# Kernel optimization log

Measured on AMD Instinct MI355X. Metric: run time of the kernel, lower is better.

The kernel has to match this reference:

```python
import jax, jax.numpy as jnp
import numpy as np

N = 50000   # nodes
E = 800000  # edges (avg degree 16)
H = 4       # attention heads
NEG_SLOPE = 0.2


def gatv2_conv(h, src, dst, W, attn, act):
    """One DGL-style GATv2Conv with share_weights=True, no bias/residual.
    h: [N, Fin]; W: [Fin, H*D]; attn: [H, D].
    """
    n = h.shape[0]
    Hh, D = attn.shape
    feat = (h @ W).reshape(n, Hh, D)          # shared src/dst projection
    el = feat[src]                             # [E, H, D] gathered source feats
    er = feat[dst]                             # [E, H, D] gathered dest feats
    # GATv2 score: a^T leaky_relu(W h_i + W h_j)
    e = jnp.sum(jax.nn.leaky_relu(el + er, NEG_SLOPE) * attn, axis=-1)  # [E, H]
    # edge softmax over incoming edges of each destination node
    m = jax.ops.segment_max(e, dst, num_segments=n)        # [N, H]
    ex = jnp.exp(e - m[dst])                                # stable exp
    s = jax.ops.segment_sum(ex, dst, num_segments=n)        # [N, H]
    a = ex / s[dst]                                         # [E, H]
    # weighted scatter-sum of source features
    rst = jax.ops.segment_sum(el * a[:, :, None], dst, num_segments=n)  # [N, H, D]
    return act(rst) if act is not None else rst


def setup_inputs() -> dict:
    key = jax.random.key(0)
    ks = jax.random.split(key, 12)
    p = lambda k, shape: (jax.random.normal(k, shape, jnp.float32) * 0.1)
    return {
        "features": jax.random.normal(ks[0], (N, 16), jnp.float32),
        "W0": p(ks[3], (16, H * 32)),  "attn0": p(ks[4], (H, 32)),
        "W1": p(ks[5], (H * 32, H * 32)), "attn1": p(ks[6], (H, 32)),
        "W2": p(ks[7], (H * 32, H * 32)), "attn2": p(ks[8], (H, 32)),
        "W3": p(ks[9], (H * 32, H * 8)),  "attn3": p(ks[10], (H, 8)),
        "src": jax.random.randint(ks[1], (E,), 0, N, jnp.int32),
        "dst": jax.random.randint(ks[2], (E,), 0, N, jnp.int32),
    }


def reference(features, W0, attn0, W1, attn1, W2, attn2, W3, attn3, src, dst):
    h = gatv2_conv(features, src, dst, W0, attn0, jax.nn.elu).reshape(N, -1)
    h = gatv2_conv(h, src, dst, W1, attn1, jax.nn.elu).reshape(N, -1)
    h = gatv2_conv(h, src, dst, W2, attn2, jax.nn.elu).reshape(N, -1)
    logits = gatv2_conv(h, src, dst, W3, attn3, None).mean(axis=1)  # [N, num_classes]
    return logits
```

## Files before the change

### kernel.cpp

```cpp
#include <hip/hip_runtime.h>
#include <hip/hip_bf16.h>
#include <math.h>

#define N_NODES 50000
#define N_EDGES 800000
#define HEADS 4
#define NEG 0.2f

#define SCAN_TILE 1024
#define SCAN_NB ((N_NODES + SCAN_TILE - 1) / SCAN_TILE)

template<int FIN>
__global__ __launch_bounds__(256) void gemm128_kernel(const float* __restrict__ h,
                                                      const float* __restrict__ W,
                                                      float* __restrict__ out) {
    constexpr int ROWS = 32;
    __shared__ float hs[ROWS][FIN];
    const int tid = threadIdx.x;
    const int rbase = blockIdx.x * ROWS;
    constexpr int VECS = ROWS * FIN / 4;
    for (int i = tid; i < VECS; i += 256) {
        int r = (i * 4) / FIN, c = (i * 4) % FIN;
        int gr = rbase + r;
        float4 v = {0.f, 0.f, 0.f, 0.f};
        if (gr < N_NODES) v = *(const float4*)(h + (size_t)gr * FIN + c);
        *(float4*)(&hs[r][c]) = v;
    }
    __syncthreads();
    const int c4 = (tid & 31) * 4;
    const int r0 = (tid >> 5) * 4;
    float a0[4] = {}, a1[4] = {}, a2[4] = {}, a3[4] = {};
    for (int k = 0; k < FIN; ++k) {
        const float4 w = *(const float4*)(W + k * 128 + c4);
        const float h0 = hs[r0 + 0][k], h1 = hs[r0 + 1][k];
        const float h2 = hs[r0 + 2][k], h3 = hs[r0 + 3][k];
        a0[0] += h0 * w.x; a0[1] += h0 * w.y; a0[2] += h0 * w.z; a0[3] += h0 * w.w;
        a1[0] += h1 * w.x; a1[1] += h1 * w.y; a1[2] += h1 * w.z; a1[3] += h1 * w.w;
        a2[0] += h2 * w.x; a2[1] += h2 * w.y; a2[2] += h2 * w.z; a2[3] += h2 * w.w;
        a3[0] += h3 * w.x; a3[1] += h3 * w.y; a3[2] += h3 * w.z; a3[3] += h3 * w.w;
    }
    float* rows[4] = {a0, a1, a2, a3};
#pragma unroll
    for (int i = 0; i < 4; ++i) {
        int gr = rbase + r0 + i;
        if (gr < N_NODES) {
            float4 v = {rows[i][0], rows[i][1], rows[i][2], rows[i][3]};
            *(float4*)(out + (size_t)gr * 128 + c4) = v;
        }
    }
}

template<int FIN, int FOUT>
__global__ __launch_bounds__(128) void gemm_kernel(const float* __restrict__ h,
                                                   const float* __restrict__ W,
                                                   float* __restrict__ out) {
    constexpr int ROWS = 16;
    constexpr int SUBS = 128 / FOUT;
    constexpr int RPT  = ROWS / SUBS;
    __shared__ float hs[ROWS][FIN];
    const int tid = threadIdx.x;
    const int rbase = blockIdx.x * ROWS;
    for (int i = tid; i < ROWS * FIN; i += 128) {
        int r = i / FIN, c = i % FIN;
        int gr = rbase + r;
        hs[r][c] = (gr < N_NODES) ? h[(size_t)gr * FIN + c] : 0.f;
    }
    __syncthreads();
    const int col = tid % FOUT;
    const int sub = tid / FOUT;
    float acc[RPT];
#pragma unroll
    for (int i = 0; i < RPT; ++i) acc[i] = 0.f;
    for (int k = 0; k < FIN; ++k) {
        float w = W[k * FOUT + col];
#pragma unroll
        for (int i = 0; i < RPT; ++i) acc[i] += hs[sub * RPT + i][k] * w;
    }
#pragma unroll
    for (int i = 0; i < RPT; ++i) {
        int gr = rbase + sub * RPT + i;
        if (gr < N_NODES) out[(size_t)gr * FOUT + col] = acc[i];
    }
}

__global__ __launch_bounds__(256) void deg_count(const int* __restrict__ dst,
                                                 int* __restrict__ deg) {
    int e = blockIdx.x * blockDim.x + threadIdx.x;
    if (e < N_EDGES) atomicAdd(&deg[dst[e]], 1);
}

__global__ __launch_bounds__(256) void scan_reduce(const int* __restrict__ deg,
                                                   int* __restrict__ bsum) {
    __shared__ int wtot[4];
    const int tid = threadIdx.x;
    const int base = blockIdx.x * SCAN_TILE + tid * 4;
    int s = 0;
    if (base < N_NODES) {
        int4 v = *(const int4*)(deg + base);
        s = v.x + v.y + v.z + v.w;
    }
#pragma unroll
    for (int off = 1; off < 64; off <<= 1) s += __shfl_xor(s, off, 64);
    if ((tid & 63) == 0) wtot[tid >> 6] = s;
    __syncthreads();
    if (tid == 0) bsum[blockIdx.x] = wtot[0] + wtot[1] + wtot[2] + wtot[3];
}

__global__ __launch_bounds__(256) void scan_write(const int* __restrict__ deg,
                                                  const int* __restrict__ bsum,
                                                  int* __restrict__ row_ptr,
                                                  int* __restrict__ woff) {
    __shared__ int s_boff;
    __shared__ int wtot[4];
    const int tid  = threadIdx.x;
    const int lane = tid & 63;
    const int wid  = tid >> 6;
    const int b    = blockIdx.x;
    if (wid == 0) {
        int v = (lane < b) ? bsum[lane] : 0;
#pragma unroll
        for (int off = 1; off < 64; off <<= 1) v += __shfl_xor(v, off, 64);
        if (lane == 0) s_boff = v;
    }
    const int base = b * SCAN_TILE + tid * 4;
    int4 v = {0, 0, 0, 0};
    if (base < N_NODES) v = *(const int4*)(deg + base);
    const int t0 = v.x, t1 = t0 + v.y, t2 = t1 + v.z, t3 = t2 + v.w;
    int x = t3;
#pragma unroll
    for (int off = 1; off < 64; off <<= 1) {
        int t = __shfl_up(x, off, 64);
        if (lane >= off) x += t;
    }
    if (lane == 63) wtot[wid] = x;
    __syncthreads();
    int woffs = 0;
    for (int w = 0; w < wid; ++w) woffs += wtot[w];
    const int off0 = s_boff + woffs + (x - t3);
    if (base < N_NODES) {
        row_ptr[base + 1] = off0 + t0;  woff[base + 0] = off0 + t0 - v.x;
        row_ptr[base + 2] = off0 + t1;  woff[base + 1] = off0 + t1 - v.y;
        row_ptr[base + 3] = off0 + t2;  woff[base + 2] = off0 + t2 - v.z;
        row_ptr[base + 4] = off0 + t3;  woff[base + 3] = off0 + t3 - v.w;
    }
    if (b == 0 && tid == 0) row_ptr[0] = 0;
}

__global__ __launch_bounds__(256) void scatter_kernel(const int* __restrict__ src,
                                                      const int* __restrict__ dst,
                                                      int* __restrict__ woff,
                                                      int* __restrict__ csr_src) {
    int e = blockIdx.x * blockDim.x + threadIdx.x;
    if (e < N_EDGES) {
        int pos = atomicAdd(&woff[dst[e]], 1);
        csr_src[pos] = src[e];
    }
}

template<int D, int MODE>
__global__ __launch_bounds__(256) void fused_gat(const float* __restrict__ feat,
                                                 const int* __restrict__ row_ptr,
                                                 const int* __restrict__ csr_src,
                                                 const float* __restrict__ attn,
                                                 float* __restrict__ out) {
    constexpr int F   = HEADS * D;
    constexpr int LPN = F / 4;
    constexpr int NPW = 64 / LPN;
    const int lane = threadIdx.x & 63;
    const int wave = (blockIdx.x * blockDim.x + threadIdx.x) >> 6;
    const int sub  = lane / LPN;
    const int l    = lane % LPN;
    const int v    = wave * NPW + sub;
    if (v >= N_NODES) return;

    const float4 a4 = *(const float4*)(attn + (l * 4));
    const float4 fv = *(const float4*)(feat + (size_t)v * F + l * 4);

    float m = -INFINITY, s = 0.f;
    float4 acc = {0.f, 0.f, 0.f, 0.f};

    const int beg = row_ptr[v], end = row_ptr[v + 1];
    int j = beg;
    for (; j + 1 < end; j += 2) {
        const int u0 = csr_src[j], u1 = csr_src[j + 1];
        const float4 f0 = *(const float4*)(feat + (size_t)u0 * F + l * 4);
        const float4 f1 = *(const float4*)(feat + (size_t)u1 * F + l * 4);
        float t, sc0 = 0.f, sc1 = 0.f;
        t = f0.x + fv.x; t = t > 0.f ? t : t * NEG; sc0 += t * a4.x;
        t = f0.y + fv.y; t = t > 0.f ? t : t * NEG; sc0 += t * a4.y;
        t = f0.z + fv.z; t = t > 0.f ? t : t * NEG; sc0 += t * a4.z;
        t = f0.w + fv.w; t = t > 0.f ? t : t * NEG; sc0 += t * a4.w;
        t = f1.x + fv.x; t = t > 0.f ? t : t * NEG; sc1 += t * a4.x;
        t = f1.y + fv.y; t = t > 0.f ? t : t * NEG; sc1 += t * a4.y;
        t = f1.z + fv.z; t = t > 0.f ? t : t * NEG; sc1 += t * a4.z;
        t = f1.w + fv.w; t = t > 0.f ? t : t * NEG; sc1 += t * a4.w;
#pragma unroll
        for (int off = 1; off < D / 4; off <<= 1) {
            sc0 += __shfl_xor(sc0, off, 64);
            sc1 += __shfl_xor(sc1, off, 64);
        }
        const float scmax = fmaxf(sc0, sc1);
        if (scmax > m) {
            const float scale = __expf(m - scmax);
            s *= scale;
            acc.x *= scale; acc.y *= scale; acc.z *= scale; acc.w *= scale;
            m = scmax;
        }
        const float p0 = __expf(sc0 - m);
        const float p1 = __expf(sc1 - m);
        s += p0 + p1;
        acc.x += f0.x * p0 + f1.x * p1;
        acc.y += f0.y * p0 + f1.y * p1;
        acc.z += f0.z * p0 + f1.z * p1;
        acc.w += f0.w * p0 + f1.w * p1;
    }
    if (j < end) {
        const int u = csr_src[j];
        const float4 fu = *(const float4*)(feat + (size_t)u * F + l * 4);
        float t, sc = 0.f;
        t = fu.x + fv.x; t = t > 0.f ? t : t * NEG; sc += t * a4.x;
        t = fu.y + fv.y; t = t > 0.f ? t : t * NEG; sc += t * a4.y;
        t = fu.z + fv.z; t = t > 0.f ? t : t * NEG; sc += t * a4.z;
        t = fu.w + fv.w; t = t > 0.f ? t : t * NEG; sc += t * a4.w;
#pragma unroll
        for (int off = 1; off < D / 4; off <<= 1)
            sc += __shfl_xor(sc, off, 64);
        if (sc > m) {
            const float scale = __expf(m - sc);
            s *= scale;
            acc.x *= scale; acc.y *= scale; acc.z *= scale; acc.w *= scale;
            m = sc;
        }
        const float p = __expf(sc - m);
        s += p;
        acc.x += fu.x * p;
        acc.y += fu.y * p;
        acc.z += fu.z * p;
        acc.w += fu.w * p;
    }

    const float inv = (s > 0.f) ? 1.f / s : 0.f;
    float4 r;
    r.x = acc.x * inv; r.y = acc.y * inv; r.z = acc.z * inv; r.w = acc.w * inv;
    if (MODE == 0) {
        r.x = r.x > 0.f ? r.x : expm1f(r.x);
        r.y = r.y > 0.f ? r.y : expm1f(r.y);
        r.z = r.z > 0.f ? r.z : expm1f(r.z);
        r.w = r.w > 0.f ? r.w : expm1f(r.w);
        *(float4*)(out + (size_t)v * F + l * 4) = r;
    } else {
        r.x += __shfl_xor(r.x, 2, 64); r.y += __shfl_xor(r.y, 2, 64);
        r.z += __shfl_xor(r.z, 2, 64); r.w += __shfl_xor(r.w, 2, 64);
        r.x += __shfl_xor(r.x, 4, 64); r.y += __shfl_xor(r.y, 4, 64);
        r.z += __shfl_xor(r.z, 4, 64); r.w += __shfl_xor(r.w, 4, 64);
        if (l < 2) {
            r.x *= 0.25f; r.y *= 0.25f; r.z *= 0.25f; r.w *= 0.25f;
            *(float4*)(out + (size_t)v * 8 + l * 4) = r;
        }
    }
}

extern "C" void kernel_launch(void* const* d_in, const int* in_sizes, int n_in,
                              void* d_out, int out_size, void* d_ws, size_t ws_size,
                              hipStream_t stream) {
    const float* features = (const float*)d_in[0];
    const float* W0 = (const float*)d_in[1];  const float* attn0 = (const float*)d_in[2];
    const float* W1 = (const float*)d_in[3];  const float* attn1 = (const float*)d_in[4];
    const float* W2 = (const float*)d_in[5];  const float* attn2 = (const float*)d_in[6];
    const float* W3 = (const float*)d_in[7];  const float* attn3 = (const float*)d_in[8];
    const int* src = (const int*)d_in[9];
    const int* dst = (const int*)d_in[10];
    float* out = (float*)d_out;

    float* bufA   = (float*)d_ws;
    float* feat   = bufA + (size_t)N_NODES * 128;
    int* row_ptr  = (int*)(feat + (size_t)N_NODES * 128);
    int* woff     = row_ptr + (N_NODES + 1);
    int* deg      = woff + N_NODES;
    int* csr_src  = deg + N_NODES;
    int* bsum     = csr_src + N_EDGES;

    const int EBLK = (N_EDGES + 255) / 256;
    const int GB32 = (N_NODES + 31) / 32;
    const int GB16 = (N_NODES + 15) / 16;

    hipMemsetAsync(deg, 0, (size_t)N_NODES * 4, stream);
    deg_count<<<EBLK, 256, 0, stream>>>(dst, deg);
    scan_reduce<<<SCAN_NB, 256, 0, stream>>>(deg, bsum);
    scan_write<<<SCAN_NB, 256, 0, stream>>>(deg, bsum, row_ptr, woff);
    scatter_kernel<<<EBLK, 256, 0, stream>>>(src, dst, woff, csr_src);

    const int FB32 = ((N_NODES + 1) / 2 * 64 + 255) / 256;
    const int FB8  = ((N_NODES + 7) / 8 * 64 + 255) / 256;

    gemm128_kernel<16><<<GB32, 256, 0, stream>>>(features, W0, feat);
    fused_gat<32, 0><<<FB32, 256, 0, stream>>>(feat, row_ptr, csr_src, attn0, bufA);
    gemm128_kernel<128><<<GB32, 256, 0, stream>>>(bufA, W1, feat);
    fused_gat<32, 0><<<FB32, 256, 0, stream>>>(feat, row_ptr, csr_src, attn1, bufA);
    gemm128_kernel<128><<<GB32, 256, 0, stream>>>(bufA, W2, feat);
    fused_gat<32, 0><<<FB32, 256, 0, stream>>>(feat, row_ptr, csr_src, attn2, bufA);
    gemm_kernel<128, 32><<<GB16, 128, 0, stream>>>(bufA, W3, feat);
    fused_gat<8, 1><<<FB8, 256, 0, stream>>>(feat, row_ptr, csr_src, attn3, out);
}
```

Baseline: 467.9 us.

## Assign one wavefront per node and split edges across sub-slots with online-softmax merge

Each node now gets a full 64-lane wavefront instead of sharing one. The lanes are split into edge-parallel slots that each process a strided subset of incoming edges with unrolled loads. Partial online-softmax states (max, sum, accumulator) are then merged across slots with xor shuffles, and only slot 0 writes. The aim is more memory-level parallelism and shorter serial edge chains per node. In exchange it uses 2x (D=32) or 8x (D=8) more waves, plus extra merge shuffles and exps.

```diff
diff --git a/kernel.cpp b/kernel.cpp
--- a/kernel.cpp
+++ b/kernel.cpp
@@ -163,97 +163,113 @@
                                                  const int* __restrict__ csr_src,
                                                  const float* __restrict__ attn,
                                                  float* __restrict__ out) {
-    constexpr int F   = HEADS * D;
-    constexpr int LPN = F / 4;
-    constexpr int NPW = 64 / LPN;
+    constexpr int F    = HEADS * D;
+    constexpr int LPN  = F / 4;
+    constexpr int EPAR = 64 / LPN;
+    constexpr int UNR  = (D == 32) ? 4 : 2;
+    constexpr int CHUNK = EPAR * UNR;
     const int lane = threadIdx.x & 63;
-    const int wave = (blockIdx.x * blockDim.x + threadIdx.x) >> 6;
-    const int sub  = lane / LPN;
+    const int v    = (blockIdx.x * blockDim.x + threadIdx.x) >> 6;
+    if (v >= N_NODES) return;
+    const int slot = lane / LPN;
     const int l    = lane % LPN;
-    const int v    = wave * NPW + sub;
-    if (v >= N_NODES) return;
-
-    const float4 a4 = *(const float4*)(attn + (l * 4));
+
+    const float4 a4 = *(const float4*)(attn + l * 4);
     const float4 fv = *(const float4*)(feat + (size_t)v * F + l * 4);
 
     float m = -INFINITY, s = 0.f;
     float4 acc = {0.f, 0.f, 0.f, 0.f};
 
     const int beg = row_ptr[v], end = row_ptr[v + 1];
-    int j = beg;
-    for (; j + 1 < end; j += 2) {
-        const int u0 = csr_src[j], u1 = csr_src[j + 1];
-        const float4 f0 = *(const float4*)(feat + (size_t)u0 * F + l * 4);
-        const float4 f1 = *(const float4*)(feat + (size_t)u1 * F + l * 4);
-        float t, sc0 = 0.f, sc1 = 0.f;
-        t = f0.x + fv.x; t = t > 0.f ? t : t * NEG; sc0 += t * a4.x;
-        t = f0.y + fv.y; t = t > 0.f ? t : t * NEG; sc0 += t * a4.y;
-        t = f0.z + fv.z; t = t > 0.f ? t : t * NEG; sc0 += t * a4.z;
-        t = f0.w + fv.w; t = t > 0.f ? t : t * NEG; sc0 += t * a4.w;
-        t = f1.x + fv.x; t = t > 0.f ? t : t * NEG; sc1 += t * a4.x;
-        t = f1.y + fv.y; t = t > 0.f ? t : t * NEG; sc1 += t * a4.y;
-        t = f1.z + fv.z; t = t > 0.f ? t : t * NEG; sc1 += t * a4.z;
-        t = f1.w + fv.w; t = t > 0.f ? t : t * NEG; sc1 += t * a4.w;
+    for (int jc = beg; jc < end; jc += CHUNK) {
+        int    idx[UNR];
+        bool   act[UNR];
+        float4 fr[UNR];
+        float  sc[UNR];
+#pragma unroll
+        for (int u = 0; u < UNR; ++u) {
+            const int j = jc + u * EPAR + slot;
+            act[u] = (j < end);
+            idx[u] = act[u] ? csr_src[j] : v;
+        }
+#pragma unroll
+        for (int u = 0; u < UNR; ++u)
+            fr[u] = *(const float4*)(feat + (size_t)idx[u] * F + l * 4);
+#pragma unroll
+        for (int u = 0; u < UNR; ++u) {
+            float t, x;
+            t = fr[u].x + fv.x; t = t > 0.f ? t : t * NEG; x  = t * a4.x;
+            t = fr[u].y + fv.y; t = t > 0.f ? t : t * NEG; x += t * a4.y;
+            t = fr[u].z + fv.z; t = t > 0.f ? t : t * NEG; x += t * a4.z;
+            t = fr[u].w + fv.w; t = t > 0.f ? t : t * NEG; x += t * a4.w;
+            sc[u] = x;
+        }
 #pragma unroll
         for (int off = 1; off < D / 4; off <<= 1) {
-            sc0 += __shfl_xor(sc0, off, 64);
-            sc1 += __shfl_xor(sc1, off, 64);
-        }
-        const float scmax = fmaxf(sc0, sc1);
+#pragma unroll
+            for (int u = 0; u < UNR; ++u)
+                sc[u] += __shfl_xor(sc[u], off, 64);
+        }
+#pragma unroll
+        for (int u = 0; u < UNR; ++u)
+            if (!act[u]) sc[u] = -INFINITY;
+        float scmax = sc[0];
+#pragma unroll
+        for (int u = 1; u < UNR; ++u) scmax = fmaxf(scmax, sc[u]);
         if (scmax > m) {
             const float scale = __expf(m - scmax);
             s *= scale;
             acc.x *= scale; acc.y *= scale; acc.z *= scale; acc.w *= scale;
             m = scmax;
         }
-        const float p0 = __expf(sc0 - m);
-        const float p1 = __expf(sc1 - m);
-        s += p0 + p1;
-        acc.x += f0.x * p0 + f1.x * p1;
-        acc.y += f0.y * p0 + f1.y * p1;
-        acc.z += f0.z * p0 + f1.z * p1;
-        acc.w += f0.w * p0 + f1.w * p1;
-    }
-    if (j < end) {
-        const int u = csr_src[j];
-        const float4 fu = *(const float4*)(feat + (size_t)u * F + l * 4);
-        float t, sc = 0.f;
-        t = fu.x + fv.x; t = t > 0.f ? t : t * NEG; sc += t * a4.x;
-        t = fu.y + fv.y; t = t > 0.f ? t : t * NEG; sc += t * a4.y;
-        t = fu.z + fv.z; t = t > 0.f ? t : t * NEG; sc += t * a4.z;
-        t = fu.w + fv.w; t = t > 0.f ? t : t * NEG; sc += t * a4.w;
-#pragma unroll
-        for (int off = 1; off < D / 4; off <<= 1)
-            sc += __shfl_xor(sc, off, 64);
-        if (sc > m) {
-            const float scale = __expf(m - sc);
-            s *= scale;
-            acc.x *= scale; acc.y *= scale; acc.z *= scale; acc.w *= scale;
-            m = sc;
-        }
-        const float p = __expf(sc - m);
-        s += p;
-        acc.x += fu.x * p;
-        acc.y += fu.y * p;
-        acc.z += fu.z * p;
-        acc.w += fu.w * p;
+#pragma unroll
+        for (int u = 0; u < UNR; ++u) {
+            const float p = act[u] ? __expf(sc[u] - m) : 0.f;
+            s += p;
+            acc.x += fr[u].x * p;
+            acc.y += fr[u].y * p;
+            acc.z += fr[u].z * p;
+            acc.w += fr[u].w * p;
+        }
+    }
+
+#pragma unroll
+    for (int off = LPN; off < 64; off <<= 1) {
+        const float mo = __shfl_xor(m, off, 64);
+        const float so = __shfl_xor(s, off, 64);
+        float4 ao;
+        ao.x = __shfl_xor(acc.x, off, 64);
+        ao.y = __shfl_xor(acc.y, off, 64);
+        ao.z = __shfl_xor(acc.z, off, 64);
+        ao.w = __shfl_xor(acc.w, off, 64);
+        const float mM = fmaxf(m, mo);
+        const float f  = (m  < mM) ? __expf(m  - mM) : 1.f;
+        const float fo = (mo < mM) ? __expf(mo - mM) : 1.f;
+        s = s * f + so * fo;
+        acc.x = acc.x * f + ao.x * fo;
+        acc.y = acc.y * f + ao.y * fo;
+        acc.z = acc.z * f + ao.z * fo;
+        acc.w = acc.w * f + ao.w * fo;
+        m = mM;
     }
 
     const float inv = (s > 0.f) ? 1.f / s : 0.f;
     float4 r;
     r.x = acc.x * inv; r.y = acc.y * inv; r.z = acc.z * inv; r.w = acc.w * inv;
     if (MODE == 0) {
-        r.x = r.x > 0.f ? r.x : expm1f(r.x);
-        r.y = r.y > 0.f ? r.y : expm1f(r.y);
-        r.z = r.z > 0.f ? r.z : expm1f(r.z);
-        r.w = r.w > 0.f ? r.w : expm1f(r.w);
-        *(float4*)(out + (size_t)v * F + l * 4) = r;
+        if (slot == 0) {
+            r.x = r.x > 0.f ? r.x : expm1f(r.x);
+            r.y = r.y > 0.f ? r.y : expm1f(r.y);
+            r.z = r.z > 0.f ? r.z : expm1f(r.z);
+            r.w = r.w > 0.f ? r.w : expm1f(r.w);
+            *(float4*)(out + (size_t)v * F + l * 4) = r;
+        }
     } else {
         r.x += __shfl_xor(r.x, 2, 64); r.y += __shfl_xor(r.y, 2, 64);
         r.z += __shfl_xor(r.z, 2, 64); r.w += __shfl_xor(r.w, 2, 64);
         r.x += __shfl_xor(r.x, 4, 64); r.y += __shfl_xor(r.y, 4, 64);
         r.z += __shfl_xor(r.z, 4, 64); r.w += __shfl_xor(r.w, 4, 64);
-        if (l < 2) {
+        if (slot == 0 && l < 2) {
             r.x *= 0.25f; r.y *= 0.25f; r.z *= 0.25f; r.w *= 0.25f;
             *(float4*)(out + (size_t)v * 8 + l * 4) = r;
         }
@@ -290,15 +306,14 @@
     scan_write<<<SCAN_NB, 256, 0, stream>>>(deg, bsum, row_ptr, woff);
     scatter_kernel<<<EBLK, 256, 0, stream>>>(src, dst, woff, csr_src);
 
-    const int FB32 = ((N_NODES + 1) / 2 * 64 + 255) / 256;
-    const int FB8  = ((N_NODES + 7) / 8 * 64 + 255) / 256;
+    const int FB = ((size_t)N_NODES * 64 + 255) / 256;
 
     gemm128_kernel<16><<<GB32, 256, 0, stream>>>(features, W0, feat);
-    fused_gat<32, 0><<<FB32, 256, 0, stream>>>(feat, row_ptr, csr_src, attn0, bufA);
+    fused_gat<32, 0><<<FB, 256, 0, stream>>>(feat, row_ptr, csr_src, attn0, bufA);
     gemm128_kernel<128><<<GB32, 256, 0, stream>>>(bufA, W1, feat);
-    fused_gat<32, 0><<<FB32, 256, 0, stream>>>(feat, row_ptr, csr_src, attn1, bufA);
+    fused_gat<32, 0><<<FB, 256, 0, stream>>>(feat, row_ptr, csr_src, attn1, bufA);
     gemm128_kernel<128><<<GB32, 256, 0, stream>>>(bufA, W2, feat);
-    fused_gat<32, 0><<<FB32, 256, 0, stream>>>(feat, row_ptr, csr_src, attn2, bufA);
+    fused_gat<32, 0><<<FB, 256, 0, stream>>>(feat, row_ptr, csr_src, attn2, bufA);
     gemm_kernel<128, 32><<<GB16, 128, 0, stream>>>(bufA, W3, feat);
-    fused_gat<8, 1><<<FB8, 256, 0, stream>>>(feat, row_ptr, csr_src, attn3, out);
-}
+    fused_gat<8, 1><<<FB, 256, 0, stream>>>(feat, row_ptr, csr_src, attn3, out);
+}
```

Measured after the change: 470.9 us. Within noise of the previous version (+0.6%).
